# Optimization experiments

Hardware: AMD Instinct MI355X
Metric: run time of the kernel (lower is better)

Reference implementation:

```python
import jax, jax.numpy as jnp
import numpy as np

# MalConv-style dims: byte vocab, tiny embed, wide stride-=kernel gated conv
B, T, V, E, C, K, S, N = 8, 1048576, 257, 8, 128, 512, 512, 64


def setup_inputs() -> dict:
    key = jax.random.key(0)
    k1, k2, k3, k4 = jax.random.split(key, 4)
    x = jax.random.randint(k1, (B, T), 0, V, dtype=jnp.int32)
    emb = jax.random.normal(k2, (V, E), dtype=jnp.float32) * 0.02
    fan = 1.0 / np.sqrt(E * K)
    w1 = jax.random.normal(k3, (C, E, K), dtype=jnp.float32) * fan
    w2 = jax.random.normal(k4, (C, E, K), dtype=jnp.float32) * fan
    b1 = jnp.zeros((C,), jnp.float32)
    b2 = jnp.zeros((C,), jnp.float32)
    return {"x": x, "emb": emb, "w1": w1, "b1": b1, "w2": w2, "b2": b2}


def reference(x, emb, w1, b1, w2, b2):
    # preprocess: byte embedding -> (B, E, T)
    z = emb[x].transpose(0, 2, 1)
    dn = ("NCH", "OIH", "NCH")
    # GatedConvolution: c1 * sigmoid(c2), valid conv, stride S -> (B, C, L)
    c1 = jax.lax.conv_general_dilated(z, w1, (S,), "VALID", dimension_numbers=dn) + b1[None, :, None]
    c2 = jax.lax.conv_general_dilated(z, w2, (S,), "VALID", dimension_numbers=dn) + b2[None, :, None]
    g = c1 * jax.nn.sigmoid(c2)  # (B, C, L)
    L = g.shape[-1]
    # input-space position of each conv output window; patch assignment
    pos = jnp.arange(L, dtype=jnp.int32) * S
    patch_size = -(-T // N)  # ceil(T / num_patches)
    seg = jnp.clip(pos // patch_size, 0, N - 1)  # (L,)
    # per-patch max-over-time, per channel: segment_max over the L axis
    gl = g.transpose(2, 0, 1).reshape(L, B * C)  # (L, B*C)
    mv = jax.ops.segment_max(gl, seg, num_segments=N)  # (N, B*C)
    max_vals = mv.reshape(N, B, C).transpose(1, 0, 2)  # (B, N, C)
    return max_vals
```

## Files before the change

### kernel.cpp

```cpp
#include <hip/hip_runtime.h>
#include <hip/hip_bf16.h>
#include <math.h>


typedef __bf16 bf16x8 __attribute__((ext_vector_type(8)));
typedef float  f32x4  __attribute__((ext_vector_type(4)));

#define WS_WP_OFF   0
#define WS_EMB_OFF  (2u << 20)
#define WS_C_OFF    (4u << 20)

__device__ __forceinline__ void load_lds16(const void* g, void* l) {
    __builtin_amdgcn_global_load_lds(
        (const __attribute__((address_space(1))) void*)g,
        (__attribute__((address_space(3))) void*)l,
        16, 0, 0);
}

__global__ void prep_kernel(const float* __restrict__ w1,
                            const float* __restrict__ w2,
                            const float* __restrict__ emb,
                            uint4* __restrict__ Wp4,
                            __bf16* __restrict__ embp) {
    int bid = blockIdx.x;
    int tid = threadIdx.x;
    if (bid < 128) {
        __shared__ __bf16 lds[8192];
        int cb = bid & 7;
        int sB = bid >> 3;
        int c0 = cb << 5;
        const float* wsrc = (c0 < 128) ? (w1 + ((size_t)c0 << 12))
                                       : (w2 + ((size_t)(c0 - 128) << 12));
        int j4  = tid & 7;
        int pr0 = tid >> 3;
#pragma unroll
        for (int p = 0; p < 8; ++p) {
            int pair = p * 32 + pr0;
            int cl = pair >> 3, e = pair & 7;
            const float4 v = *(const float4*)(wsrc + (cl << 12) + (e << 9) + (sB << 5) + (j4 << 2));
            float vv[4] = {v.x, v.y, v.z, v.w};
#pragma unroll
            for (int jj = 0; jj < 4; ++jj) {
                int j = (j4 << 2) + jj;
                int qq = j >> 3, tt = j & 7;
                lds[(((qq << 3) + tt) * 32 + cl) * 8 + e] = (__bf16)vv[jj];
            }
        }
        __syncthreads();
        const uint4* l4 = (const uint4*)lds;
        int nhalf = cb & 1, nt = cb >> 1;
        int base = (nt << 15) + (sB << 11) + (nhalf << 5);
#pragma unroll
        for (int it = 0; it < 4; ++it) {
            int idx = it * 256 + tid;
            int qq = idx >> 8, tt = (idx >> 5) & 7, w = idx & 31;
            Wp4[base + (tt << 8) + (qq << 6) + w] = l4[idx];
        }
    } else {
        for (int i = tid; i < 2056; i += 256) embp[i] = (__bf16)emb[i];
    }
}

__global__ __launch_bounds__(256, 2)
void gemm_kernel(const int* __restrict__ x,
                 const __bf16* __restrict__ Wp,
                 const uint4* __restrict__ embp,
                 float* __restrict__ Cbuf,
                 int ksplit) {
    __shared__ uint4 ldsB[2][2048];
    __shared__ uint4 embl[257];

    const int tid  = threadIdx.x;
    const int wave = tid >> 6;
    const int lane = tid & 63;
    const int q    = lane >> 4;
    const int nl   = lane & 15;

    for (int i = tid; i < 257; i += 256) embl[i] = embp[i];

    const int bid = blockIdx.x;
    int mt, nt, kh, nsteps, s0;
    if (ksplit == 2) {
        mt = ((bid >> 6) << 3) | (bid & 7);
        int combo = (bid >> 3) & 7;
        kh = combo & 1; nt = combo >> 1;
        nsteps = 8; s0 = kh << 3;
    } else {
        mt = ((bid >> 5) << 3) | (bid & 7);
        nt = (bid >> 3) & 3;
        kh = 0; nsteps = 16; s0 = 0;
    }
    const int m0 = mt << 8;
    const int rA = m0 + (wave << 6) + nl;
    const char* WpBase = (const char*)Wp + ((size_t)nt << 19);

    const int* xp[4];
#pragma unroll
    for (int rg = 0; rg < 4; ++rg)
        xp[rg] = x + (size_t)(rA + (rg << 4)) * 512 + (q << 3);

    int4 xc[4][2];
#pragma unroll
    for (int rg = 0; rg < 4; ++rg) {
        const int* p = xp[rg] + (s0 << 5);
        xc[rg][0] = *(const int4*)p;
        xc[rg][1] = *(const int4*)(p + 4);
    }
    {
        const char* src = WpBase + ((size_t)s0 << 15) + tid * 16;
        char* dst = (char*)&ldsB[0][0] + tid * 16;
#pragma unroll
        for (int i = 0; i < 8; ++i) load_lds16(src + i * 4096, dst + i * 4096);
    }
    __syncthreads();

    f32x4 acc[4][4] = {};

    for (int ss = 0; ss < nsteps; ++ss) {
        const int sp  = s0 + ss;
        const int buf = ss & 1;
        if (ss + 1 < nsteps) {
            const char* src = WpBase + ((size_t)(sp + 1) << 15) + tid * 16;
            char* dst = (char*)&ldsB[buf ^ 1][0] + tid * 16;
#pragma unroll
            for (int i = 0; i < 8; ++i) load_lds16(src + i * 4096, dst + i * 4096);
        }
        int idx[4][8];
#pragma unroll
        for (int rg = 0; rg < 4; ++rg) {
            idx[rg][0] = xc[rg][0].x; idx[rg][1] = xc[rg][0].y;
            idx[rg][2] = xc[rg][0].z; idx[rg][3] = xc[rg][0].w;
            idx[rg][4] = xc[rg][1].x; idx[rg][5] = xc[rg][1].y;
            idx[rg][6] = xc[rg][1].z; idx[rg][7] = xc[rg][1].w;
        }
        const int spn = (ss + 1 < nsteps) ? sp + 1 : sp;
#pragma unroll
        for (int rg = 0; rg < 4; ++rg) {
            const int* p = xp[rg] + (spn << 5);
            xc[rg][0] = *(const int4*)p;
            xc[rg][1] = *(const int4*)(p + 4);
        }
        const char* Bbase = (const char*)&ldsB[buf][0] + (q << 10) + (nl << 4);
#pragma unroll
        for (int t = 0; t < 8; ++t) {
            bf16x8 a[4];
#pragma unroll
            for (int rg = 0; rg < 4; ++rg)
                a[rg] = *reinterpret_cast<const bf16x8*>(&embl[idx[rg][t]]);
#pragma unroll
            for (int nf = 0; nf < 4; ++nf) {
                bf16x8 b = *reinterpret_cast<const bf16x8*>(Bbase + (t << 12) + (nf << 8));
#pragma unroll
                for (int rg = 0; rg < 4; ++rg)
                    acc[rg][nf] = __builtin_amdgcn_mfma_f32_16x16x32_bf16(a[rg], b, acc[rg][nf], 0, 0, 0);
            }
        }
        __syncthreads();
    }

    float* Cout = Cbuf + (size_t)kh * (16384 * 256);
#pragma unroll
    for (int rg = 0; rg < 4; ++rg) {
        int rowb = m0 + (wave << 6) + (rg << 4) + (q << 2);
#pragma unroll
        for (int nf = 0; nf < 4; ++nf) {
            int col = (nt << 6) + (nf << 4) + nl;
#pragma unroll
            for (int i = 0; i < 4; ++i)
                Cout[(size_t)(rowb + i) * 256 + col] = acc[rg][nf][i];
        }
    }
}

__global__ void reduce_kernel(const float* __restrict__ Cbuf,
                              const float* __restrict__ b1,
                              const float* __restrict__ b2,
                              float* __restrict__ out,
                              int ksplit) {
    __shared__ float sm[256];
    int tid = threadIdx.x;
    int c   = tid & 127;
    int lh  = tid >> 7;
    int gp  = blockIdx.x;
    float bb1 = b1[c], bb2 = b2[c];
    const float* base0 = Cbuf + (size_t)(gp * 32 + lh * 16) * 256 + c;
    const float* base1 = base0 + (size_t)16384 * 256;
    const bool ks2 = (ksplit == 2);
    float best = -INFINITY;
#pragma unroll 4
    for (int l = 0; l < 16; ++l) {
        float c1 = base0[0]   + bb1;
        float c2 = base0[128] + bb2;
        if (ks2) { c1 += base1[0]; c2 += base1[128]; }
        float g = c1 * (1.0f / (1.0f + __expf(-c2)));
        best = fmaxf(best, g);
        base0 += 256; base1 += 256;
    }
    sm[tid] = best;
    __syncthreads();
    if (lh == 0) out[(size_t)gp * 128 + c] = fmaxf(sm[tid], sm[tid + 128]);
}

extern "C" void kernel_launch(void* const* d_in, const int* in_sizes, int n_in,
                              void* d_out, int out_size, void* d_ws, size_t ws_size,
                              hipStream_t stream) {
    const int*   x   = (const int*)d_in[0];
    const float* emb = (const float*)d_in[1];
    const float* w1  = (const float*)d_in[2];
    const float* b1  = (const float*)d_in[3];
    const float* w2  = (const float*)d_in[4];
    const float* b2  = (const float*)d_in[5];
    float* out = (float*)d_out;

    char* ws = (char*)d_ws;
    __bf16* Wp   = (__bf16*)(ws + WS_WP_OFF);
    __bf16* embp = (__bf16*)(ws + WS_EMB_OFF);
    float*  Cbuf = (float*)(ws + WS_C_OFF);

    const size_t need2 = (size_t)(4u << 20) + 2ull * 16384 * 256 * 4;
    int ksplit = (ws_size >= need2) ? 2 : 1;

    prep_kernel<<<129, 256, 0, stream>>>(w1, w2, emb, (uint4*)Wp, embp);
    gemm_kernel<<<256 * ksplit, 256, 0, stream>>>(x, Wp, (const uint4*)embp, Cbuf, ksplit);
    reduce_kernel<<<512, 256, 0, stream>>>(Cbuf, b1, b2, out, ksplit);
}
```

Before: 124.0 us.

## Pack byte indices to u16 in MFMA order and widen GEMM N-tile with 4-way K split

Adds a prep_x kernel that narrows the int32 byte indices to uint16 and lays them out in the exact per-lane order the MFMA loop consumes. The GEMM tile grows from 64 to 128 columns (c1 or c2 half per block) and K is split four ways, so each embedding gather feeds more MFMAs and the index loads become contiguous vector loads. The reduce kernel is rewritten to sum four partial buffers with vector loads and staging through LDS. The trade-offs are an extra kernel launch, a larger workspace requirement with the ws_size fallback removed, and more partial-sum traffic, plus higher register pressure from the doubled accumulator set.

```diff
diff --git a/kernel.cpp b/kernel.cpp
--- a/kernel.cpp
+++ b/kernel.cpp
@@ -6,9 +6,10 @@
 typedef __bf16 bf16x8 __attribute__((ext_vector_type(8)));
 typedef float  f32x4  __attribute__((ext_vector_type(4)));
 
-#define WS_WP_OFF   0
+#define WS_WP_OFF   0u
 #define WS_EMB_OFF  (2u << 20)
-#define WS_C_OFF    (4u << 20)
+#define WS_XP_OFF   (4u << 20)
+#define WS_C_OFF    (24u << 20)
 
 __device__ __forceinline__ void load_lds16(const void* g, void* l) {
     __builtin_amdgcn_global_load_lds(
@@ -17,157 +18,152 @@
         16, 0, 0);
 }
 
-__global__ void prep_kernel(const float* __restrict__ w1,
-                            const float* __restrict__ w2,
-                            const float* __restrict__ emb,
-                            uint4* __restrict__ Wp4,
-                            __bf16* __restrict__ embp) {
-    int bid = blockIdx.x;
-    int tid = threadIdx.x;
-    if (bid < 128) {
-        __shared__ __bf16 lds[8192];
-        int cb = bid & 7;
-        int sB = bid >> 3;
-        int c0 = cb << 5;
-        const float* wsrc = (c0 < 128) ? (w1 + ((size_t)c0 << 12))
-                                       : (w2 + ((size_t)(c0 - 128) << 12));
-        int j4  = tid & 7;
-        int pr0 = tid >> 3;
-#pragma unroll
-        for (int p = 0; p < 8; ++p) {
-            int pair = p * 32 + pr0;
-            int cl = pair >> 3, e = pair & 7;
-            const float4 v = *(const float4*)(wsrc + (cl << 12) + (e << 9) + (sB << 5) + (j4 << 2));
+__global__ void prep_w(const float* __restrict__ w1,
+                       const float* __restrict__ w2,
+                       const float* __restrict__ emb,
+                       uint4* __restrict__ Wp4,
+                       __bf16* __restrict__ embp) {
+    int bid = blockIdx.x, tid = threadIdx.x;
+    if (bid < 64) {
+        __shared__ __bf16 lds[16384];
+        int nt = bid >> 5, sg = bid & 31;
+        const float* wsrc = nt ? w2 : w1;
+#pragma unroll
+        for (int i = 0; i < 16; ++i) {
+            int g = i * 256 + tid;
+            int j4 = g & 3, pair = g >> 2;
+            int e = pair & 7, cl = pair >> 3;
+            float4 v = *(const float4*)(wsrc + cl * 4096 + e * 512 + sg * 16 + j4 * 4);
             float vv[4] = {v.x, v.y, v.z, v.w};
 #pragma unroll
-            for (int jj = 0; jj < 4; ++jj) {
-                int j = (j4 << 2) + jj;
-                int qq = j >> 3, tt = j & 7;
-                lds[(((qq << 3) + tt) * 32 + cl) * 8 + e] = (__bf16)vv[jj];
-            }
+            for (int jj = 0; jj < 4; ++jj)
+                lds[(cl * 16 + j4 * 4 + jj) * 8 + e] = (__bf16)vv[jj];
         }
         __syncthreads();
         const uint4* l4 = (const uint4*)lds;
-        int nhalf = cb & 1, nt = cb >> 1;
-        int base = (nt << 15) + (sB << 11) + (nhalf << 5);
-#pragma unroll
-        for (int it = 0; it < 4; ++it) {
-            int idx = it * 256 + tid;
-            int qq = idx >> 8, tt = (idx >> 5) & 7, w = idx & 31;
-            Wp4[base + (tt << 8) + (qq << 6) + w] = l4[idx];
+#pragma unroll
+        for (int it = 0; it < 8; ++it) {
+            int j = it * 256 + tid;
+            int n = j & 127, q = (j >> 7) & 3, tt = (j >> 9) & 3;
+            Wp4[bid * 2048 + j] = l4[n * 16 + tt * 4 + q];
         }
     } else {
         for (int i = tid; i < 2056; i += 256) embp[i] = (__bf16)emb[i];
     }
 }
 
+__global__ void prep_x(const int* __restrict__ x,
+                       unsigned short* __restrict__ xp) {
+    __shared__ unsigned short lds[256 * 136];
+    int bid = blockIdx.x, tid = threadIdx.x;
+    int mt = bid >> 2, kh = bid & 3;
+    const long src0 = (long)mt * 131072 + kh * 128;
+#pragma unroll
+    for (int i = 0; i < 32; ++i) {
+        int f = i * 256 + tid;
+        int row = f >> 5, c = (f & 31) * 4;
+        int4 v = *(const int4*)(x + src0 + (long)row * 512 + c);
+        ushort4 s;
+        s.x = (unsigned short)v.x; s.y = (unsigned short)v.y;
+        s.z = (unsigned short)v.z; s.w = (unsigned short)v.w;
+        *(ushort4*)&lds[row * 136 + c] = s;
+    }
+    __syncthreads();
+    unsigned short* dst = xp + (size_t)bid * 32768;
+#pragma unroll
+    for (int i = 0; i < 32; ++i) {
+        int jc = i * 256 + tid;
+        int rg = jc & 3, lane = (jc >> 2) & 63, wv = (jc >> 8) & 3, st = jc >> 10;
+        int q = lane >> 4, nl = lane & 15;
+        int row = wv * 64 + rg * 16 + nl;
+        int cb = st * 16 + q;
+        ushort4 s;
+        s.x = lds[row * 136 + cb];
+        s.y = lds[row * 136 + cb + 4];
+        s.z = lds[row * 136 + cb + 8];
+        s.w = lds[row * 136 + cb + 12];
+        *(ushort4*)&dst[jc * 4] = s;
+    }
+}
+
 __global__ __launch_bounds__(256, 2)
-void gemm_kernel(const int* __restrict__ x,
+void gemm_kernel(const unsigned short* __restrict__ xp,
                  const __bf16* __restrict__ Wp,
                  const uint4* __restrict__ embp,
-                 float* __restrict__ Cbuf,
-                 int ksplit) {
+                 float* __restrict__ Cbuf) {
     __shared__ uint4 ldsB[2][2048];
     __shared__ uint4 embl[257];
 
-    const int tid  = threadIdx.x;
-    const int wave = tid >> 6;
-    const int lane = tid & 63;
-    const int q    = lane >> 4;
-    const int nl   = lane & 15;
+    const int tid = threadIdx.x;
+    const int wv = tid >> 6, lane = tid & 63;
+    const int q = lane >> 4, nl = lane & 15;
 
     for (int i = tid; i < 257; i += 256) embl[i] = embp[i];
 
     const int bid = blockIdx.x;
-    int mt, nt, kh, nsteps, s0;
-    if (ksplit == 2) {
-        mt = ((bid >> 6) << 3) | (bid & 7);
-        int combo = (bid >> 3) & 7;
-        kh = combo & 1; nt = combo >> 1;
-        nsteps = 8; s0 = kh << 3;
-    } else {
-        mt = ((bid >> 5) << 3) | (bid & 7);
-        nt = (bid >> 3) & 3;
-        kh = 0; nsteps = 16; s0 = 0;
-    }
+    const int mt = bid >> 3, nt = bid & 1, kh = (bid >> 1) & 3;
     const int m0 = mt << 8;
-    const int rA = m0 + (wave << 6) + nl;
-    const char* WpBase = (const char*)Wp + ((size_t)nt << 19);
-
-    const int* xp[4];
-#pragma unroll
-    for (int rg = 0; rg < 4; ++rg)
-        xp[rg] = x + (size_t)(rA + (rg << 4)) * 512 + (q << 3);
-
-    int4 xc[4][2];
-#pragma unroll
-    for (int rg = 0; rg < 4; ++rg) {
-        const int* p = xp[rg] + (s0 << 5);
-        xc[rg][0] = *(const int4*)p;
-        xc[rg][1] = *(const int4*)(p + 4);
-    }
+
+    const char* WpBase = (const char*)Wp + (size_t)(nt * 32 + kh * 8) * 32768;
+    const unsigned short* xpS = xp + (size_t)(mt * 4 + kh) * 32768 + (wv * 64 + lane) * 16;
+
     {
-        const char* src = WpBase + ((size_t)s0 << 15) + tid * 16;
-        char* dst = (char*)&ldsB[0][0] + tid * 16;
-#pragma unroll
-        for (int i = 0; i < 8; ++i) load_lds16(src + i * 4096, dst + i * 4096);
-    }
-    __syncthreads();
-
-    f32x4 acc[4][4] = {};
-
-    for (int ss = 0; ss < nsteps; ++ss) {
-        const int sp  = s0 + ss;
-        const int buf = ss & 1;
-        if (ss + 1 < nsteps) {
-            const char* src = WpBase + ((size_t)(sp + 1) << 15) + tid * 16;
-            char* dst = (char*)&ldsB[buf ^ 1][0] + tid * 16;
-#pragma unroll
-            for (int i = 0; i < 8; ++i) load_lds16(src + i * 4096, dst + i * 4096);
-        }
-        int idx[4][8];
-#pragma unroll
-        for (int rg = 0; rg < 4; ++rg) {
-            idx[rg][0] = xc[rg][0].x; idx[rg][1] = xc[rg][0].y;
-            idx[rg][2] = xc[rg][0].z; idx[rg][3] = xc[rg][0].w;
-            idx[rg][4] = xc[rg][1].x; idx[rg][5] = xc[rg][1].y;
-            idx[rg][6] = xc[rg][1].z; idx[rg][7] = xc[rg][1].w;
-        }
-        const int spn = (ss + 1 < nsteps) ? sp + 1 : sp;
-#pragma unroll
-        for (int rg = 0; rg < 4; ++rg) {
-            const int* p = xp[rg] + (spn << 5);
-            xc[rg][0] = *(const int4*)p;
-            xc[rg][1] = *(const int4*)(p + 4);
-        }
-        const char* Bbase = (const char*)&ldsB[buf][0] + (q << 10) + (nl << 4);
-#pragma unroll
-        for (int t = 0; t < 8; ++t) {
+        const char* src = WpBase + tid * 16;
+        char* dstl = (char*)&ldsB[0][0] + tid * 16;
+#pragma unroll
+        for (int i = 0; i < 8; ++i) load_lds16(src + i * 4096, dstl + i * 4096);
+    }
+    uint4 xa = *(const uint4*)(xpS);
+    uint4 xb = *(const uint4*)(xpS + 8);
+    __syncthreads();
+
+    f32x4 acc[4][8] = {};
+
+    for (int st = 0; st < 8; ++st) {
+        const int buf = st & 1;
+        uint4 xa_n = xa, xb_n = xb;
+        if (st < 7) {
+            const char* src = WpBase + (size_t)(st + 1) * 32768 + tid * 16;
+            char* dstl = (char*)&ldsB[buf ^ 1][0] + tid * 16;
+#pragma unroll
+            for (int i = 0; i < 8; ++i) load_lds16(src + i * 4096, dstl + i * 4096);
+            const unsigned short* xn = xpS + (size_t)(st + 1) * 4096;
+            xa_n = *(const uint4*)(xn);
+            xb_n = *(const uint4*)(xn + 8);
+        }
+        const unsigned int u[8] = {xa.x, xa.y, xa.z, xa.w, xb.x, xb.y, xb.z, xb.w};
+#pragma unroll
+        for (int tt = 0; tt < 4; ++tt) {
             bf16x8 a[4];
 #pragma unroll
-            for (int rg = 0; rg < 4; ++rg)
-                a[rg] = *reinterpret_cast<const bf16x8*>(&embl[idx[rg][t]]);
-#pragma unroll
-            for (int nf = 0; nf < 4; ++nf) {
-                bf16x8 b = *reinterpret_cast<const bf16x8*>(Bbase + (t << 12) + (nf << 8));
+            for (int rg = 0; rg < 4; ++rg) {
+                unsigned int w = u[rg * 2 + (tt >> 1)];
+                int idx = (tt & 1) ? (int)(w >> 16) : (int)(w & 0xffffu);
+                a[rg] = *reinterpret_cast<const bf16x8*>(&embl[idx]);
+            }
+            const char* Bb = (const char*)&ldsB[buf][0] + (((tt * 4 + q) * 128 + nl) << 4);
+#pragma unroll
+            for (int nf = 0; nf < 8; ++nf) {
+                bf16x8 b = *reinterpret_cast<const bf16x8*>(Bb + nf * 256);
 #pragma unroll
                 for (int rg = 0; rg < 4; ++rg)
                     acc[rg][nf] = __builtin_amdgcn_mfma_f32_16x16x32_bf16(a[rg], b, acc[rg][nf], 0, 0, 0);
             }
         }
+        xa = xa_n; xb = xb_n;
         __syncthreads();
     }
 
-    float* Cout = Cbuf + (size_t)kh * (16384 * 256);
+    float* Cp = Cbuf + (size_t)kh * 4194304;
 #pragma unroll
     for (int rg = 0; rg < 4; ++rg) {
-        int rowb = m0 + (wave << 6) + (rg << 4) + (q << 2);
-#pragma unroll
-        for (int nf = 0; nf < 4; ++nf) {
-            int col = (nt << 6) + (nf << 4) + nl;
+        int rowb = m0 + wv * 64 + rg * 16 + q * 4;
+#pragma unroll
+        for (int nf = 0; nf < 8; ++nf) {
+            int col = nt * 128 + nf * 16 + nl;
 #pragma unroll
             for (int i = 0; i < 4; ++i)
-                Cout[(size_t)(rowb + i) * 256 + col] = acc[rg][nf][i];
+                Cp[(size_t)(rowb + i) * 256 + col] = acc[rg][nf][i];
         }
     }
 }
@@ -175,30 +171,52 @@
 __global__ void reduce_kernel(const float* __restrict__ Cbuf,
                               const float* __restrict__ b1,
                               const float* __restrict__ b2,
-                              float* __restrict__ out,
-                              int ksplit) {
-    __shared__ float sm[256];
-    int tid = threadIdx.x;
-    int c   = tid & 127;
-    int lh  = tid >> 7;
-    int gp  = blockIdx.x;
-    float bb1 = b1[c], bb2 = b2[c];
-    const float* base0 = Cbuf + (size_t)(gp * 32 + lh * 16) * 256 + c;
-    const float* base1 = base0 + (size_t)16384 * 256;
-    const bool ks2 = (ksplit == 2);
-    float best = -INFINITY;
-#pragma unroll 4
-    for (int l = 0; l < 16; ++l) {
-        float c1 = base0[0]   + bb1;
-        float c2 = base0[128] + bb2;
-        if (ks2) { c1 += base1[0]; c2 += base1[128]; }
-        float g = c1 * (1.0f / (1.0f + __expf(-c2)));
-        best = fmaxf(best, g);
-        base0 += 256; base1 += 256;
-    }
-    sm[tid] = best;
-    __syncthreads();
-    if (lh == 0) out[(size_t)gp * 128 + c] = fmaxf(sm[tid], sm[tid + 128]);
+                              float* __restrict__ out) {
+    __shared__ f32x4 smC[32 * 64];
+    __shared__ f32x4 smM[8 * 32];
+    int tid = threadIdx.x, gp = blockIdx.x;
+    size_t base = (size_t)gp * 32 * 256;
+#pragma unroll
+    for (int i = 0; i < 8; ++i) {
+        int t = i * 256 + tid;
+        int row = t >> 6, c4 = t & 63;
+        f32x4 s = {};
+#pragma unroll
+        for (int kh = 0; kh < 4; ++kh) {
+            f32x4 v = *(const f32x4*)(Cbuf + (size_t)kh * 4194304 + base + row * 256 + c4 * 4);
+            s += v;
+        }
+        smC[row * 64 + c4] = s;
+    }
+    __syncthreads();
+    int c4 = tid & 31, rgp = tid >> 5;
+    f32x4 bb1 = *(const f32x4*)(b1 + c4 * 4);
+    f32x4 bb2 = *(const f32x4*)(b2 + c4 * 4);
+    f32x4 m;
+    m[0] = m[1] = m[2] = m[3] = -INFINITY;
+#pragma unroll
+    for (int r = 0; r < 4; ++r) {
+        int row = rgp * 4 + r;
+        f32x4 a = smC[row * 64 + c4];
+        f32x4 b = smC[row * 64 + c4 + 32];
+#pragma unroll
+        for (int j = 0; j < 4; ++j) {
+            float g = (a[j] + bb1[j]) * (1.0f / (1.0f + __expf(-(b[j] + bb2[j]))));
+            m[j] = fmaxf(m[j], g);
+        }
+    }
+    smM[rgp * 32 + c4] = m;
+    __syncthreads();
+    if (tid < 32) {
+        f32x4 mm = smM[tid];
+#pragma unroll
+        for (int r = 1; r < 8; ++r) {
+            f32x4 v = smM[r * 32 + tid];
+#pragma unroll
+            for (int j = 0; j < 4; ++j) mm[j] = fmaxf(mm[j], v[j]);
+        }
+        *(f32x4*)(out + gp * 128 + tid * 4) = mm;
+    }
 }
 
 extern "C" void kernel_launch(void* const* d_in, const int* in_sizes, int n_in,
@@ -213,14 +231,13 @@
     float* out = (float*)d_out;
 
     char* ws = (char*)d_ws;
-    __bf16* Wp   = (__bf16*)(ws + WS_WP_OFF);
-    __bf16* embp = (__bf16*)(ws + WS_EMB_OFF);
-    float*  Cbuf = (float*)(ws + WS_C_OFF);
-
-    const size_t need2 = (size_t)(4u << 20) + 2ull * 16384 * 256 * 4;
-    int ksplit = (ws_size >= need2) ? 2 : 1;
-
-    prep_kernel<<<129, 256, 0, stream>>>(w1, w2, emb, (uint4*)Wp, embp);
-    gemm_kernel<<<256 * ksplit, 256, 0, stream>>>(x, Wp, (const uint4*)embp, Cbuf, ksplit);
-    reduce_kernel<<<512, 256, 0, stream>>>(Cbuf, b1, b2, out, ksplit);
-}
+    __bf16*         Wp   = (__bf16*)(ws + WS_WP_OFF);
+    __bf16*         embp = (__bf16*)(ws + WS_EMB_OFF);
+    unsigned short* xpp  = (unsigned short*)(ws + WS_XP_OFF);
+    float*          Cbuf = (float*)(ws + WS_C_OFF);
+
+    prep_w<<<65, 256, 0, stream>>>(w1, w2, emb, (uint4*)Wp, embp);
+    prep_x<<<256, 256, 0, stream>>>(x, xpp);
+    gemm_kernel<<<512, 256, 0, stream>>>(xpp, Wp, (const uint4*)embp, Cbuf);
+    reduce_kernel<<<512, 256, 0, stream>>>(Cbuf, b1, b2, out);
+}
```

New measurement: 141.5 us. +14.1%, slower.
